# Performance work log

Measured on AMD Instinct MI355X. Metric: run time of the kernel, lower is better.

Reference implementation:

```python
import jax, jax.numpy as jnp
import numpy as np

B, S, D = 128, 50, 128
NUM_NODE = 40000
HOP, N_ITER, SAMPLE = 2, 2, 12
N_NEI = 8
TEMP, MU, LEAK = 0.5, 0.1, 0.2


def setup_inputs() -> dict:
    key = jax.random.key(0)
    ks = jax.random.split(key, 32)
    stdv = 1.0 / np.sqrt(D)
    u = lambda k, shp: jax.random.uniform(k, shp, jnp.float32, -stdv, stdv)
    return {
        "inputs": jax.random.randint(ks[0], (B, S), 0, NUM_NODE),
        "adj": jax.random.randint(ks[1], (B, S, S), 0, 5),
        "item": jax.random.randint(ks[2], (B, S), 0, NUM_NODE),
        "simi_mask": jax.random.randint(ks[3], (B, S, S), 0, 2),
        "as_items_0": jax.random.randint(ks[4], (B, S, N_NEI), 0, NUM_NODE),
        "as_items_1": jax.random.randint(ks[5], (B, S, N_NEI), 0, NUM_NODE),
        "as_items_ssl_0": jax.random.randint(ks[6], (B, S, N_NEI), 0, NUM_NODE),
        "as_items_ssl_1": jax.random.randint(ks[7], (B, S, N_NEI), 0, NUM_NODE),
        "last_item_mask": jnp.zeros((B, S), bool).at[:, -1].set(True),
        "adj_all": jax.random.randint(ks[8], (NUM_NODE, SAMPLE), 0, NUM_NODE),
        "num": jax.random.uniform(ks[9], (NUM_NODE, SAMPLE)),
        "emb": u(ks[10], (NUM_NODE, D)),
        "pos_emb": u(ks[11], (200, D)),
        "a_local": u(ks[12], (N_ITER, 4, D)),
        "mir_w1": u(ks[13], (N_ITER, D, D)),
        "mir_w2": u(ks[14], (N_ITER, D, D)),
        "glob_w1": u(ks[15], (HOP, D + 1, D)),
        "glob_w2": u(ks[16], (HOP, D, 1)),
        "glob_w3": u(ks[17], (HOP, 2 * D, D)),
        "attr_w": u(ks[18], (2 * D, D)),
        "highway_w": u(ks[19], (2 * D, D)),
        "glu1_w": u(ks[20], (D, D)),
        "glu2_w": u(ks[21], (D, D)),
        "glu4_w": u(ks[22], (D, D)),
        "glu4_b": u(ks[23], (D,)),
        "w_s": u(ks[24], (D, 1)),
        "gate_w": u(ks[25], (2 * D, D)),
    }


def _forward(num, emb, pos_emb, a_local, mir_w1, mir_w2, glob_w1, glob_w2, glob_w3,
             attr_w, highway_w, glu1_w, glu2_w, glu4_w, glu4_b, w_s, gate_w,
             inputs, adj, item, simi_mask, as_lists, as_ssl_lists, last_item_mask, adj_all):
    mi = (inputs != 0).astype(emb.dtype)  # [B,S]
    h = emb[inputs]                        # [B,S,D]

    # ---- AttributeAggregator (masked-mean pool per attribute + gated fusion) ----
    def pool(idx_list):
        ps = []
        for idx in idx_list:
            m = (idx != 0).astype(emb.dtype)[..., None]  # [B,S,N,1]
            ps.append(jnp.sum(emb[idx] * m, 2) / (jnp.sum(m, 2) + 1e-8))
        return jnp.mean(jnp.stack(ps), 0)  # [B,S,D]
    hf1 = pool(as_lists)
    hf2 = pool(as_ssl_lists)
    g_attr = jax.nn.sigmoid(jnp.concatenate([h, hf1], -1) @ attr_w)
    hf = g_attr * h + (1.0 - g_attr) * hf1

    # ---- multi-hop neighbor sampling (irregular gathers) ----
    neigh = [inputs]
    wts = []
    for _ in range(HOP):
        flat = neigh[-1].reshape(-1)
        neigh.append(adj_all[flat].reshape(B, -1))
        wts.append(num[flat].reshape(B, -1))
    ev = [emb[n] for n in neigh]  # [B,S,D], [B,S*12,D], [B,S*144,D]

    item_emb = emb[item] * mi[..., None]
    sess = jnp.sum(item_emb, 1) / jnp.sum(mi, -1, keepdims=True)  # [B,D]

    # ---- GlobalAggregator stack (GCE-GNN style attention over sampled neighbors) ----
    for n_hop in range(HOP):
        nxt = []
        for hop in range(HOP - n_hop):
            sv = ev[hop]                                   # [B,M,D]
            nv = ev[hop + 1].reshape(B, -1, SAMPLE, D)     # [B,M,12,D]
            nw = wts[hop].reshape(B, -1, SAMPLE)           # [B,M,12]
            extra = jnp.broadcast_to(sess[:, None, None, :], nv.shape)
            a = jnp.concatenate([extra * nv, nw[..., None]], -1)  # [B,M,12,D+1]
            a = jax.nn.leaky_relu(a @ glob_w1[n_hop], LEAK)
            a = jax.nn.softmax((a @ glob_w2[n_hop])[..., 0], -1)[..., None]
            agg = jnp.sum(a * nv, -2)
            nxt.append(jnp.tanh(jnp.concatenate([sv, agg], -1) @ glob_w3[n_hop]))
        ev = nxt
    h_global = ev[0].reshape(B, S, D)

    # ---- LocalAggregator (edge-typed GAT) + MirrorAggregator (gated exchange) ----
    x = h
    mirror = hf
    for i in range(HOP):
        e = jax.nn.leaky_relu(jnp.einsum('bid,bjd,kd->kbij', x, x, a_local[i]), LEAK)
        att = jnp.full((B, S, S), -9e15, x.dtype)
        for k in range(4):
            att = jnp.where(adj == k + 1, e[k], att)
        x = jax.nn.softmax(att, -1) @ x
        gm = jax.nn.sigmoid(x @ mir_w1[i] + mirror @ mir_w2[i])
        x, mirror = gm * x + (1.0 - gm) * mirror, gm * mirror + (1.0 - gm) * x

    # ---- highway + last-item select ----
    g = jax.nn.sigmoid(jnp.concatenate([h, x], -1) @ highway_w)
    x_dot = g * h + (1.0 - g) * x
    h_local = jnp.sum(x_dot * last_item_mask[..., None].astype(x_dot.dtype), 1)  # [B,D]

    mask = mi[..., None]
    pos = pos_emb[:S][None]  # [1,S,D]
    bw = emb[1:]             # [NUM_NODE-1,D]
    hs = jnp.sum(h_global * mask, -2) / jnp.sum(mask, 1)  # [B,D]

    # ---- SSL pairwise similarity loss ----
    sim = jnp.einsum('bid,bjd->bij', hf1, hf2) / TEMP
    l = -jnp.log(jax.nn.softmax(sim, 2) + 1e-8)
    simi_loss = jnp.mean(jnp.sum(l * (simi_mask == 1), (1, 2)))

    # ---- attention-style GLU scoring ----
    hp = x_dot + pos
    nh = jax.nn.sigmoid(hp @ glu1_w + hs[:, None, :] @ glu2_w + h_local[:, None, :] @ glu4_w + glu4_b)
    beta = (nh @ w_s) * mask
    zg = jnp.sum(beta * hp, 1)  # [B,D]
    gf = jax.nn.sigmoid(jnp.concatenate([zg, h_local], -1) @ gate_w) * MU
    zh = gf * h_local + (1.0 - gf) * zg
    scores = zh @ bw.T  # [B, NUM_NODE-1]
    return simi_loss, scores


def reference(inputs, adj, item, simi_mask, as_items_0, as_items_1,
              as_items_ssl_0, as_items_ssl_1, last_item_mask, adj_all, num,
              emb, pos_emb, a_local, mir_w1, mir_w2, glob_w1, glob_w2, glob_w3,
              attr_w, highway_w, glu1_w, glu2_w, glu4_w, glu4_b, w_s, gate_w):
    return _forward(num, emb, pos_emb, a_local, mir_w1, mir_w2, glob_w1, glob_w2, glob_w3,
                    attr_w, highway_w, glu1_w, glu2_w, glu4_w, glu4_b, w_s, gate_w,
                    inputs, adj, item, simi_mask, [as_items_0, as_items_1],
                    [as_items_ssl_0, as_items_ssl_1], last_item_mask, adj_all)
```

## Files before the change

kernel.cpp:

```cpp
#include <hip/hip_runtime.h>
#include <hip/hip_bf16.h>
#include <type_traits>


#define B 128
#define S 50
#define D 128
#define SAMPLE 12
#define NNEI 8
#define NODES 40000
#define NSC (NODES - 1)
#define LEAK 0.2f
#define TEMPV 0.5f
#define MUV 0.1f
#define NEG_BIG -3.0e38f
#define NUNITS (B * S * 13)
#define NGA (NUNITS / 4)

typedef const float* fpp;
typedef float* fpw;
typedef unsigned short u16;
typedef __attribute__((ext_vector_type(8))) short bfrag8;
typedef __attribute__((ext_vector_type(4))) float f32x4;

__device__ __forceinline__ float sigm(float x) { return 1.f / (1.f + __expf(-x)); }
__device__ __forceinline__ float tanh_f(float x) { return 1.f - 2.f / (__expf(2.f * x) + 1.f); }
__device__ __forceinline__ float leaky(float x) { return x >= 0.f ? x : LEAK * x; }
__device__ __forceinline__ u16 f2bf(float v) {
  __hip_bfloat16 h = __float2bfloat16(v);
  return *reinterpret_cast<u16*>(&h);
}
__device__ __forceinline__ float lde(const float* p, long i) { return p[i]; }
__device__ __forceinline__ float lde(const u16* p, long i) {
  union { unsigned int u; float f; } c;
  c.u = ((unsigned int)p[i]) << 16;
  return c.f;
}
__device__ __forceinline__ float bfu(short s) {
  union { unsigned u; float f; } c;
  c.u = ((unsigned)(unsigned short)s) << 16;
  return c.f;
}

template <typename ET>
__device__ __forceinline__ bfrag8 load_frag(const ET* __restrict__ emb, long row, int koff) {
  if constexpr (sizeof(ET) == 2) {
    return *(const bfrag8*)(const void*)(emb + row * D + koff);
  } else {
    const float* s = (const float*)(emb + row * D + koff);
    float4 lo = *(const float4*)s;
    float4 hi = *(const float4*)(s + 4);
    bfrag8 b;
    b[0] = (short)f2bf(lo.x); b[1] = (short)f2bf(lo.y);
    b[2] = (short)f2bf(lo.z); b[3] = (short)f2bf(lo.w);
    b[4] = (short)f2bf(hi.x); b[5] = (short)f2bf(hi.y);
    b[6] = (short)f2bf(hi.z); b[7] = (short)f2bf(hi.w);
    return b;
  }
}

__device__ __forceinline__ bfrag8 scale8(bfrag8 r, float4 sa, float4 sb) {
  bfrag8 o;
  o[0] = (short)f2bf(bfu(r[0]) * sa.x); o[1] = (short)f2bf(bfu(r[1]) * sa.y);
  o[2] = (short)f2bf(bfu(r[2]) * sa.z); o[3] = (short)f2bf(bfu(r[3]) * sa.w);
  o[4] = (short)f2bf(bfu(r[4]) * sb.x); o[5] = (short)f2bf(bfu(r[5]) * sb.y);
  o[6] = (short)f2bf(bfu(r[6]) * sb.z); o[7] = (short)f2bf(bfu(r[7]) * sb.w);
  return o;
}

struct __align__(16) SMk5 { float xi[D]; float ak[4][D]; float alpha[56]; float part[4][2][64]; };
struct __align__(16) SMk7 { float hi[D]; float part[2][64]; };
struct __align__(16) SMga { u16 nvs[2][2][16 * 136]; };
struct __align__(16) SMgb {
  u16 nvs[16 * 136];
  float ev[13 * 128];
  float agg1[128];
  float red[2][16];
  float nw[16];
  int svidx[16];
};
union __align__(16) SMF1 { SMk5 a; SMk7 b; SMga c; };
union __align__(16) SMF2 { SMk5 a; SMgb d; };

__global__ __launch_bounds__(256) void kprep_emb(fpp emb, u16* __restrict__ out) {
  long i = ((long)blockIdx.x * 256 + threadIdx.x) * 4;
  if (i + 3 >= (long)NODES * D) return;
  float4 v = *(const float4*)(emb + i);
  out[i + 0] = f2bf(v.x); out[i + 1] = f2bf(v.y);
  out[i + 2] = f2bf(v.z); out[i + 3] = f2bf(v.w);
}

__global__ __launch_bounds__(256) void kprep4(fpp gw1, fpp gw3,
                                              u16* __restrict__ p1a,
                                              u16* __restrict__ p1b,
                                              u16* __restrict__ p3a,
                                              u16* __restrict__ p3b) {
  int i = blockIdx.x * 256 + threadIdx.x;
  fpp W; u16* dst; int KS;
  if (i < 16384)      { W = gw1;             dst = p1a; KS = 4; }
  else if (i < 32768) { W = gw1 + 129 * 128; dst = p1b; KS = 4; i -= 16384; }
  else if (i < 65536) { W = gw3;             dst = p3a; KS = 8; i -= 32768; }
  else                { W = gw3 + 256 * 128; dst = p3b; KS = 8; i -= 65536; }
  int e = i & 7;
  int lane = (i >> 3) & 63;
  int rest = i >> 9;
  int ks = rest % KS, nt = rest / KS;
  int k = ks * 32 + ((lane >> 4) << 3) + e;
  int n = (nt << 4) + (lane & 15);
  dst[i] = f2bf(W[(long)k * 128 + n]);
}

template <typename ET>
__global__ __launch_bounds__(128) void k1_gather(
    const int* __restrict__ inputs, const int* __restrict__ as0,
    const int* __restrict__ as1, const int* __restrict__ ss0,
    const int* __restrict__ ss1, const ET* __restrict__ emb, fpp attr_w,
    fpw h, fpw hf1, fpw hf2, float* __restrict__ mi, fpw xA, fpw mir) {
  int bs = blockIdx.x;
  int d = threadIdx.x;
  __shared__ float h_s[D], hf1_s[D];
  int inp = inputs[bs];
  float hv = lde(emb, (long)inp * D + d);
  const int* lists[4] = {as0, as1, ss0, ss1};
  float p[4];
#pragma unroll
  for (int l = 0; l < 4; l++) {
    float sum = 0.f, cnt = 0.f;
    const int* L = lists[l] + (long)bs * NNEI;
#pragma unroll
    for (int n = 0; n < NNEI; n++) {
      int idx = L[n];
      if (idx != 0) { sum += lde(emb, (long)idx * D + d); cnt += 1.f; }
    }
    p[l] = sum / (cnt + 1e-8f);
  }
  float hf1v = 0.5f * (p[0] + p[1]);
  float hf2v = 0.5f * (p[2] + p[3]);
  h_s[d] = hv;
  hf1_s[d] = hf1v;
  __syncthreads();
  float acc = 0.f;
  for (int k = 0; k < D; k++)
    acc += h_s[k] * attr_w[(long)k * D + d] + hf1_s[k] * attr_w[(long)(D + k) * D + d];
  float g = sigm(acc);
  float hfv = g * hv + (1.f - g) * hf1v;
  long o = (long)bs * D + d;
  h[o] = hv; hf1[o] = hf1v; hf2[o] = hf2v; xA[o] = hv; mir[o] = hfv;
  if (d == 0) mi[bs] = (inp != 0) ? 1.f : 0.f;
}

__global__ __launch_bounds__(128) void k2_sess(const int* __restrict__ inputs,
                                               const int* __restrict__ item,
                                               fpp emb, fpw sess) {
  int b = blockIdx.x;
  int d = threadIdx.x;
  float acc = 0.f, ms = 0.f;
  for (int s = 0; s < S; s++) {
    int inp = inputs[b * S + s];
    float m = (inp != 0) ? 1.f : 0.f;
    int it = item[b * S + s];
    acc += emb[(long)it * D + d] * m;
    ms += m;
  }
  sess[(long)b * D + d] = acc / ms;
}

template <typename ET>
__device__ __forceinline__ void dev_kga2(
    u16* __restrict__ nvs0, u16* __restrict__ nvs1,
    const int* __restrict__ inputs, const int* __restrict__ adj_all, fpp num,
    const ET* __restrict__ emb, fpp sess, fpp W1a, fpp W2a,
    const u16* __restrict__ p1a, u16* __restrict__ aggws, int gu0, int lane) {
  int q = lane >> 4;
  int mrow = lane & 15;
  float wl8[8], w28[8];
#pragma unroll
  for (int nt = 0; nt < 8; nt++) {
    int col = nt * 16 + mrow;
    wl8[nt] = W1a[(long)D * D + col];
    w28[nt] = W2a[col];
  }
  bfrag8 sA[2][4];
  float nwq[2][4];
#pragma unroll
  for (int g = 0; g < 2; g++) {
    int gu = gu0 + g;
    int bs = gu / 13;
    int u = gu - bs * 13;
    int b = bs / S;
    int src0 = inputs[bs];
    int srcu = (u == 0) ? src0 : adj_all[(long)src0 * SAMPLE + (u - 1)];
    int rid = adj_all[(long)srcu * SAMPLE + (mrow < 12 ? mrow : 0)];
#pragma unroll
    for (int i = 0; i < 4; i++)
      nwq[g][i] = (q < 3) ? num[(long)srcu * SAMPLE + q * 4 + i] : 0.f;
    const float* sessb = sess + (long)b * D;
    u16* nb = g ? nvs1 : nvs0;
    bfrag8 raw[4];
#pragma unroll
    for (int ks = 0; ks < 4; ks++)
      raw[ks] = load_frag(emb, (long)rid, ks * 32 + q * 8);
#pragma unroll
    for (int ks = 0; ks < 4; ks++)
      *(bfrag8*)(nb + mrow * 136 + ks * 32 + q * 8) = raw[ks];
#pragma unroll
    for (int ks = 0; ks < 4; ks++) {
      float4 sa = *(const float4*)(sessb + ks * 32 + q * 8);
      float4 sb = *(const float4*)(sessb + ks * 32 + q * 8 + 4);
      sA[g][ks] = scale8(raw[ks], sa, sb);
    }
  }
  float lp[2][4] = {{0.f, 0.f, 0.f, 0.f}, {0.f, 0.f, 0.f, 0.f}};
#pragma unroll
  for (int nt = 0; nt < 8; nt++) {
    f32x4 acc0 = (f32x4){0.f, 0.f, 0.f, 0.f};
    f32x4 acc1 = (f32x4){0.f, 0.f, 0.f, 0.f};
#pragma unroll
    for (int ks = 0; ks < 4; ks++) {
      bfrag8 bb = *(const bfrag8*)(p1a + ks * 512 + lane * 8 + nt * 2048);
      acc0 = __builtin_amdgcn_mfma_f32_16x16x32_bf16(sA[0][ks], bb, acc0, 0, 0, 0);
      acc1 = __builtin_amdgcn_mfma_f32_16x16x32_bf16(sA[1][ks], bb, acc1, 0, 0, 0);
    }
#pragma unroll
    for (int i = 0; i < 4; i++) {
      lp[0][i] += leaky(acc0[i] + nwq[0][i] * wl8[nt]) * w28[nt];
      lp[1][i] += leaky(acc1[i] + nwq[1][i] * wl8[nt]) * w28[nt];
    }
  }
#pragma unroll
  for (int off = 1; off <= 8; off <<= 1)
#pragma unroll
    for (int g = 0; g < 2; g++)
#pragma unroll
      for (int i = 0; i < 4; i++) lp[g][i] += __shfl_xor(lp[g][i], off, 64);
#pragma unroll
  for (int g = 0; g < 2; g++) {
    float m4 = (q < 3) ? fmaxf(fmaxf(lp[g][0], lp[g][1]), fmaxf(lp[g][2], lp[g][3]))
                       : NEG_BIG;
    m4 = fmaxf(m4, __shfl_xor(m4, 16, 64));
    m4 = fmaxf(m4, __shfl_xor(m4, 32, 64));
    float e0 = 0.f, e1 = 0.f, e2 = 0.f, e3 = 0.f, ssum = 0.f;
    if (q < 3) {
      e0 = __expf(lp[g][0] - m4); e1 = __expf(lp[g][1] - m4);
      e2 = __expf(lp[g][2] - m4); e3 = __expf(lp[g][3] - m4);
      ssum = e0 + e1 + e2 + e3;
    }
    ssum += __shfl_xor(ssum, 16, 64);
    ssum += __shfl_xor(ssum, 32, 64);
    float inv = 1.f / ssum;
    float al[4] = {e0 * inv, e1 * inv, e2 * inv, e3 * inv};
    float aj[12];
#pragma unroll
    for (int j = 0; j < 12; j++) aj[j] = __shfl(al[j & 3], (j >> 2) << 4, 64);
    const u16* nb = g ? nvs1 : nvs0;
    float a0 = 0.f, a1 = 0.f;
#pragma unroll
    for (int j = 0; j < 12; j++) {
      unsigned pv = *(const unsigned*)(nb + j * 136 + lane * 2);
      union { unsigned u; float f; } lo, hi;
      lo.u = pv << 16; hi.u = pv & 0xffff0000u;
      a0 += aj[j] * lo.f; a1 += aj[j] * hi.f;
    }
    unsigned pk = ((unsigned)f2bf(a1) << 16) | (unsigned)f2bf(a0);
    *(unsigned*)(aggws + (long)(gu0 + g) * 128 + lane * 2) = pk;
  }
}

template <typename ET>
__device__ __forceinline__ void dev_kgb(
    SMgb& sm, const int* __restrict__ inputs, const int* __restrict__ adj_all,
    fpp num, const ET* __restrict__ emb, fpp sess, fpp W1b, fpp W2b, fpp W3b,
    const u16* __restrict__ p1b, const u16* __restrict__ p3a,
    const u16* __restrict__ aggws, fpw hg, int bs) {
  int b = bs / S;
  int d = threadIdx.x;
  int lane = d & 63;
  int w = d >> 6;
  int q = lane >> 4;
  int mrow = lane & 15;

#pragma unroll
  for (int r = 12; r < 16; r++) {
    sm.nvs[r * 136 + d] = 0;
    if (d < 8) sm.nvs[r * 136 + 128 + d] = 0;
  }
  int src0 = inputs[bs];
  if (d < 16)
    sm.svidx[d] = (d == 0) ? src0 : (d <= 12 ? adj_all[(long)src0 * SAMPLE + d - 1] : 0);
  if (d < SAMPLE) sm.nw[d] = num[(long)src0 * SAMPLE + d];
  float sess_d = sess[(long)b * D + d];
  __syncthreads();

  {
    long svr = sm.svidx[mrow];
    f32x4 accB[4];
#pragma unroll
    for (int nt = 0; nt < 4; nt++) accB[nt] = (f32x4){0.f, 0.f, 0.f, 0.f};
#pragma unroll
    for (int ks = 0; ks < 4; ks++) {
      bfrag8 a = (bfrag8){0, 0, 0, 0, 0, 0, 0, 0};
      if (mrow < 13) a = load_frag(emb, svr, ks * 32 + q * 8);
      const u16* pb = p3a + (w * 32 + ks) * 512 + lane * 8;
#pragma unroll
      for (int nt = 0; nt < 4; nt++)
        accB[nt] = __builtin_amdgcn_mfma_f32_16x16x32_bf16(
            a, *(const bfrag8*)(pb + nt * 4096), accB[nt], 0, 0, 0);
    }
#pragma unroll
    for (int ks = 4; ks < 8; ks++) {
      bfrag8 a = (bfrag8){0, 0, 0, 0, 0, 0, 0, 0};
      if (mrow < 13)
        a = *(const bfrag8*)(aggws + ((long)bs * 13 + mrow) * 128 + (ks - 4) * 32 + q * 8);
      const u16* pb = p3a + (w * 32 + ks) * 512 + lane * 8;
#pragma unroll
      for (int nt = 0; nt < 4; nt++)
        accB[nt] = __builtin_amdgcn_mfma_f32_16x16x32_bf16(
            a, *(const bfrag8*)(pb + nt * 4096), accB[nt], 0, 0, 0);
    }
#pragma unroll
    for (int nt = 0; nt < 4; nt++) {
      int col = (w * 4 + nt) * 16 + mrow;
#pragma unroll
      for (int i = 0; i < 4; i++) {
        int u2 = q * 4 + i;
        if (u2 < 13) sm.ev[u2 * 128 + col] = tanh_f(accB[nt][i]);
      }
    }
  }
  __syncthreads();

  {
    float w2B[4], wlB[4];
#pragma unroll
    for (int nt = 0; nt < 4; nt++) {
      int col = (w * 4 + nt) * 16 + mrow;
      w2B[nt] = W2b[col];
      wlB[nt] = W1b[(long)D * D + col];
    }
    float evreg[SAMPLE];
#pragma unroll
    for (int j = 0; j < SAMPLE; j++) {
      float e = sm.ev[(1 + j) * 128 + d];
      evreg[j] = e;
      sm.nvs[j * 136 + d] = f2bf(e * sess_d);
    }
    __syncthreads();

    f32x4 acc[4];
#pragma unroll
    for (int nt = 0; nt < 4; nt++) acc[nt] = (f32x4){0.f, 0.f, 0.f, 0.f};
#pragma unroll
    for (int ks = 0; ks < 4; ks++) {
      bfrag8 a = *(const bfrag8*)(sm.nvs + mrow * 136 + q * 8 + ks * 32);
      const u16* pb = p1b + (w * 16 + ks) * 512 + lane * 8;
#pragma unroll
      for (int nt = 0; nt < 4; nt++) {
        bfrag8 bb = *(const bfrag8*)(pb + nt * 2048);
        acc[nt] = __builtin_amdgcn_mfma_f32_16x16x32_bf16(a, bb, acc[nt], 0, 0, 0);
      }
    }
    float lp[4] = {0.f, 0.f, 0.f, 0.f};
    float nwq[4];
#pragma unroll
    for (int i = 0; i < 4; i++) nwq[i] = (q < 3) ? sm.nw[q * 4 + i] : 0.f;
#pragma unroll
    for (int nt = 0; nt < 4; nt++)
#pragma unroll
      for (int i = 0; i < 4; i++)
        lp[i] += leaky(acc[nt][i] + nwq[i] * wlB[nt]) * w2B[nt];
#pragma unroll
    for (int off = 1; off <= 8; off <<= 1)
#pragma unroll
      for (int i = 0; i < 4; i++) lp[i] += __shfl_xor(lp[i], off, 64);
    if (mrow == 0 && q < 3) {
#pragma unroll
      for (int i = 0; i < 4; i++) sm.red[w][q * 4 + i] = lp[i];
    }
    __syncthreads();

    float lg[SAMPLE];
#pragma unroll
    for (int j = 0; j < SAMPLE; j++) lg[j] = sm.red[0][j] + sm.red[1][j];
    float mx = lg[0];
#pragma unroll
    for (int j = 1; j < SAMPLE; j++) mx = fmaxf(mx, lg[j]);
    float se = 0.f;
#pragma unroll
    for (int j = 0; j < SAMPLE; j++) { lg[j] = __expf(lg[j] - mx); se += lg[j]; }
    float inv = 1.f / se;
    float agg1d = 0.f;
#pragma unroll
    for (int j = 0; j < SAMPLE; j++) agg1d += lg[j] * inv * evreg[j];
    sm.agg1[d] = agg1d;
    __syncthreads();

    float accf = 0.f;
#pragma unroll 4
    for (int k4 = 0; k4 < 32; k4++) {
      float4 a4 = *(const float4*)&sm.ev[4 * k4];
      float4 g4 = *(const float4*)&sm.agg1[4 * k4];
      accf += a4.x * W3b[(4 * k4 + 0) * D + d] + a4.y * W3b[(4 * k4 + 1) * D + d] +
              a4.z * W3b[(4 * k4 + 2) * D + d] + a4.w * W3b[(4 * k4 + 3) * D + d] +
              g4.x * W3b[(D + 4 * k4 + 0) * D + d] + g4.y * W3b[(D + 4 * k4 + 1) * D + d] +
              g4.z * W3b[(D + 4 * k4 + 2) * D + d] + g4.w * W3b[(D + 4 * k4 + 3) * D + d];
    }
    hg[(long)bs * D + d] = tanh_f(accf);
  }
}

__device__ __forceinline__ void dev_k5ab(SMk5& sm, fpp x, const int* __restrict__ adj,
                                         fpp a_loc, fpp w1, fpp w2, fpw xout,
                                         fpw mir, fpp hw, fpp h, fpw x_dot,
                                         float* __restrict__ h_local, int bs, int fin) {
  int b = bs / S;
  int row = bs % S;
  int tid = threadIdx.x;
  long idx = ((long)b * S + row) * D + tid;
  sm.xi[tid] = x[idx];
#pragma unroll
  for (int k = 0; k < 4; k++) sm.ak[k][tid] = a_loc[(long)k * D + tid];
  __syncthreads();
  {
    int j = tid & 63, hf = tid >> 6;
    float a0 = 0.f, a1 = 0.f, a2 = 0.f, a3 = 0.f;
    if (j < S) {
      const float* xj = x + ((long)b * S + j) * D + hf * 64;
      int off = hf * 64;
      for (int dd = 0; dd < 64; dd++) {
        float prod = sm.xi[off + dd] * xj[dd];
        a0 += prod * sm.ak[0][off + dd];
        a1 += prod * sm.ak[1][off + dd];
        a2 += prod * sm.ak[2][off + dd];
        a3 += prod * sm.ak[3][off + dd];
      }
    }
    sm.part[0][hf][j] = a0; sm.part[1][hf][j] = a1;
    sm.part[2][hf][j] = a2; sm.part[3][hf][j] = a3;
  }
  __syncthreads();
  if (tid < 64) {
    int j = tid;
    float att;
    if (j < S) {
      float acc0 = sm.part[0][0][j] + sm.part[0][1][j];
      float acc1 = sm.part[1][0][j] + sm.part[1][1][j];
      float acc2 = sm.part[2][0][j] + sm.part[2][1][j];
      float acc3 = sm.part[3][0][j] + sm.part[3][1][j];
      int av = adj[((long)b * S + row) * S + j];
      att = -9e15f;
      if (av == 1) att = leaky(acc0);
      else if (av == 2) att = leaky(acc1);
      else if (av == 3) att = leaky(acc2);
      else if (av == 4) att = leaky(acc3);
    } else {
      att = NEG_BIG;
    }
    float mx = att;
#pragma unroll
    for (int o = 32; o > 0; o >>= 1) mx = fmaxf(mx, __shfl_xor(mx, o, 64));
    float e = __expf(att - mx);
    float ssum = e;
#pragma unroll
    for (int o = 32; o > 0; o >>= 1) ssum += __shfl_xor(ssum, o, 64);
    if (j < S) sm.alpha[j] = e / ssum;
  }
  __syncthreads();
  float xn = 0.f;
  for (int j = 0; j < S; j++) xn += sm.alpha[j] * x[((long)b * S + j) * D + tid];
  float mv = mir[idx];
  sm.ak[0][tid] = xn;
  sm.ak[1][tid] = mv;
  __syncthreads();
  float a2m = 0.f;
  for (int k = 0; k < D; k++)
    a2m += sm.ak[0][k] * w1[(long)k * D + tid] + sm.ak[1][k] * w2[(long)k * D + tid];
  float g = sigm(a2m);
  float xg = g * xn + (1.f - g) * mv;
  if (!fin) {
    xout[idx] = xg;
    mir[idx] = g * mv + (1.f - g) * xn;
    return;
  }
  float hv = h[idx];
  sm.ak[2][tid] = hv;
  sm.ak[3][tid] = xg;
  __syncthreads();
  float a3m = 0.f;
  for (int k = 0; k < D; k++)
    a3m += sm.ak[2][k] * hw[(long)k * D + tid] + sm.ak[3][k] * hw[(long)(D + k) * D + tid];
  float gh = sigm(a3m);
  float xd = gh * hv + (1.f - gh) * xg;
  x_dot[idx] = xd;
  if (row == S - 1) h_local[(long)b * D + tid] = xd;
}

__device__ __forceinline__ void dev_k7(SMk7& sm, fpp hf1, fpp hf2,
                                       const int* __restrict__ simi_mask,
                                       float* __restrict__ loss, int bs) {
  int b = bs / S;
  int i = bs % S;
  int t = threadIdx.x;
  sm.hi[t] = hf1[((long)b * S + i) * D + t];
  __syncthreads();
  {
    int j = t & 63, hf = t >> 6;
    float acc = 0.f;
    if (j < S) {
      const float* r = hf2 + ((long)b * S + j) * D + hf * 64;
      int off = hf * 64;
      for (int dd = 0; dd < 64; dd++) acc += sm.hi[off + dd] * r[dd];
    }
    sm.part[hf][j] = acc;
  }
  __syncthreads();
  if (t < 64) {
    int j = t;
    float sim = (j < S) ? (sm.part[0][j] + sm.part[1][j]) * (1.0f / TEMPV) : NEG_BIG;
    float mx = sim;
#pragma unroll
    for (int o = 32; o > 0; o >>= 1) mx = fmaxf(mx, __shfl_xor(mx, o, 64));
    float e = __expf(sim - mx);
    float ssum = e;
#pragma unroll
    for (int o = 32; o > 0; o >>= 1) ssum += __shfl_xor(ssum, o, 64);
    float contrib = 0.f;
    if (j < S) {
      float p = e / ssum;
      float l = -__logf(p + 1e-8f);
      if (simi_mask[((long)b * S + i) * S + j] == 1) contrib = l;
    }
#pragma unroll
    for (int o = 32; o > 0; o >>= 1) contrib += __shfl_xor(contrib, o, 64);
    if (j == 0) atomicAdd(loss, contrib);
  }
}

template <typename ET>
__global__ __launch_bounds__(128) void kF1(
    const int* __restrict__ inputs, const int* __restrict__ adj_all, fpp num,
    const ET* __restrict__ emb, fpp sess, fpp W1a, fpp W2a,
    const u16* __restrict__ p1a, u16* __restrict__ aggws,
    fpp xA, const int* __restrict__ adj, fpp a_loc, fpp mw1, fpp mw2,
    fpw xB, fpw mir,
    fpp hf1, fpp hf2, const int* __restrict__ simi_mask,
    float* __restrict__ loss) {
  __shared__ SMF1 sm;
  int bid = blockIdx.x;
  if (bid < NGA) {
    int t = threadIdx.x;
    int w = t >> 6, lane = t & 63;
    dev_kga2<ET>(sm.c.nvs[w][0], sm.c.nvs[w][1], inputs, adj_all, num, emb,
                 sess, W1a, W2a, p1a, aggws, bid * 4 + w * 2, lane);
  } else if (bid < NGA + B * S) {
    dev_k5ab(sm.a, xA, adj, a_loc, mw1, mw2, xB, mir, nullptr, nullptr,
             nullptr, nullptr, bid - NGA, 0);
  } else {
    dev_k7(sm.b, hf1, hf2, simi_mask, loss, bid - NGA - B * S);
  }
}

template <typename ET>
__global__ __launch_bounds__(128) void kF2(
    const int* __restrict__ inputs, const int* __restrict__ adj_all, fpp num,
    const ET* __restrict__ emb, fpp sess, fpp W1b, fpp W2b, fpp W3b,
    const u16* __restrict__ p1b, const u16* __restrict__ p3a,
    const u16* __restrict__ aggws, fpw hg,
    fpp xB, const int* __restrict__ adj, fpp a_loc2, fpp mw1b, fpp mw2b,
    fpw mir, fpp hw, fpp h, fpw x_dot, float* __restrict__ h_local) {
  __shared__ SMF2 sm;
  int bid = blockIdx.x;
  if (bid < B * S) {
    dev_kgb<ET>(sm.d, inputs, adj_all, num, emb, sess, W1b, W2b, W3b, p1b,
                p3a, aggws, hg, bid);
  } else {
    dev_k5ab(sm.a, xB, adj, a_loc2, mw1b, mw2b, nullptr, mir, hw, h, x_dot,
             h_local, bid - B * S, 1);
  }
}

__global__ __launch_bounds__(128) void k5ab(fpp x, const int* __restrict__ adj,
                                            fpp a_loc, fpp w1, fpp w2,
                                            fpw xout, fpw mir,
                                            fpp hw, fpp h, fpw x_dot,
                                            float* __restrict__ h_local,
                                            int fin) {
  __shared__ SMk5 sm;
  dev_k5ab(sm, x, adj, a_loc, w1, w2, xout, mir, hw, h, x_dot, h_local,
           blockIdx.x, fin);
}

__global__ __launch_bounds__(128) void k7_simi(fpp hf1, fpp hf2,
                                               const int* __restrict__ simi_mask,
                                               float* __restrict__ loss) {
  __shared__ SMk7 sm;
  dev_k7(sm, hf1, hf2, simi_mask, loss, blockIdx.x);
}

template <typename ET>
__global__ __launch_bounds__(128) void kG_mono(
    const int* __restrict__ inputs, const int* __restrict__ adj_all,
    fpp num, const ET* __restrict__ emb, fpp sess,
    fpp W1a, fpp W2a, fpp W1b, fpp W2b, fpp W3b,
    const u16* __restrict__ p1a, const u16* __restrict__ p1b,
    const u16* __restrict__ p3a, fpw hg) {
  int bs = blockIdx.x;
  int b = bs / S;
  int d = threadIdx.x;
  int lane = d & 63;
  int w = d >> 6;
  int q = lane >> 4;
  int mrow = lane & 15;

  __shared__ __align__(16) u16 nvs_l[16 * 136];
  __shared__ __align__(16) u16 svagg_l[16 * 264];
  __shared__ __align__(16) float ev_l[13 * 128];
  __shared__ __align__(16) float agg1_l[128];
  __shared__ float red_l[2][16];
  __shared__ float nw_l[16];

#pragma unroll
  for (int r = 12; r < 16; r++) {
    nvs_l[r * 136 + d] = 0;
    if (d < 8) nvs_l[r * 136 + 128 + d] = 0;
  }
#pragma unroll
  for (int r = 13; r < 16; r++) {
    svagg_l[r * 264 + d] = 0;
    svagg_l[r * 264 + 128 + d] = 0;
    if (d < 8) svagg_l[r * 264 + 256 + d] = 0;
  }

  float sess_d = sess[(long)b * D + d];
  int src0 = __builtin_amdgcn_readfirstlane(inputs[bs]);
  int n1[SAMPLE];
#pragma unroll
  for (int j = 0; j < SAMPLE; j++)
    n1[j] = __builtin_amdgcn_readfirstlane(adj_all[(long)src0 * SAMPLE + j]);
  svagg_l[0 * 264 + d] = f2bf(lde(emb, (long)src0 * D + d));

  float w2A[4], wlA[4], w2B[4], wlB[4];
#pragma unroll
  for (int nt = 0; nt < 4; nt++) {
    int col = (w * 4 + nt) * 16 + mrow;
    w2A[nt] = W2a[col];
    wlA[nt] = W1a[(long)D * D + col];
    w2B[nt] = W2b[col];
    wlB[nt] = W1b[(long)D * D + col];
  }

  float pre[SAMPLE], pnw = 0.f;
  {
#pragma unroll
    for (int j = 0; j < SAMPLE; j++)
      pre[j] = lde(emb, (long)n1[j] * D + d);
    if (d < SAMPLE) pnw = num[(long)src0 * SAMPLE + d];
  }
  for (int u = 0; u < 13; u++) {
    if (d < SAMPLE) nw_l[d] = pnw;
    float nvreg[SAMPLE];
#pragma unroll
    for (int j = 0; j < SAMPLE; j++) {
      nvreg[j] = pre[j];
      nvs_l[j * 136 + d] = f2bf(pre[j] * sess_d);
    }
    if (u == 0) {
#pragma unroll
      for (int j = 0; j < SAMPLE; j++)
        svagg_l[(1 + j) * 264 + d] = f2bf(nvreg[j]);
    }
    __syncthreads();
    if (u < 12) {
      int srcn = n1[u];
#pragma unroll
      for (int j = 0; j < SAMPLE; j++) {
        int nj = __builtin_amdgcn_readfirstlane(adj_all[(long)srcn * SAMPLE + j]);
        pre[j] = lde(emb, (long)nj * D + d);
      }
      if (d < SAMPLE) pnw = num[(long)srcn * SAMPLE + d];
    }
    f32x4 acc[4];
#pragma unroll
    for (int nt = 0; nt < 4; nt++) acc[nt] = (f32x4){0.f, 0.f, 0.f, 0.f};
#pragma unroll
    for (int ks = 0; ks < 4; ks++) {
      bfrag8 a = *(const bfrag8*)(nvs_l + mrow * 136 + q * 8 + ks * 32);
      const u16* pb = p1a + (w * 16 + ks) * 512 + lane * 8;
#pragma unroll
      for (int nt = 0; nt < 4; nt++) {
        bfrag8 bb = *(const bfrag8*)(pb + nt * 2048);
        acc[nt] = __builtin_amdgcn_mfma_f32_16x16x32_bf16(a, bb, acc[nt], 0, 0, 0);
      }
    }
    float lp[4] = {0.f, 0.f, 0.f, 0.f};
    float nwq[4];
#pragma unroll
    for (int i = 0; i < 4; i++) nwq[i] = (q < 3) ? nw_l[q * 4 + i] : 0.f;
#pragma unroll
    for (int nt = 0; nt < 4; nt++)
#pragma unroll
      for (int i = 0; i < 4; i++)
        lp[i] += leaky(acc[nt][i] + nwq[i] * wlA[nt]) * w2A[nt];
#pragma unroll
    for (int off = 1; off <= 8; off <<= 1)
#pragma unroll
      for (int i = 0; i < 4; i++) lp[i] += __shfl_xor(lp[i], off, 64);
    if (mrow == 0 && q < 3) {
#pragma unroll
      for (int i = 0; i < 4; i++) red_l[w][q * 4 + i] = lp[i];
    }
    __syncthreads();
    float lg[SAMPLE];
#pragma unroll
    for (int j = 0; j < SAMPLE; j++) lg[j] = red_l[0][j] + red_l[1][j];
    float mx = lg[0];
#pragma unroll
    for (int j = 1; j < SAMPLE; j++) mx = fmaxf(mx, lg[j]);
    float se = 0.f;
#pragma unroll
    for (int j = 0; j < SAMPLE; j++) { lg[j] = __expf(lg[j] - mx); se += lg[j]; }
    float inv = 1.f / se;
    float aggd = 0.f;
#pragma unroll
    for (int j = 0; j < SAMPLE; j++) aggd += lg[j] * inv * nvreg[j];
    svagg_l[u * 264 + 128 + d] = f2bf(aggd);
  }
  __syncthreads();

  {
    f32x4 accB[4];
#pragma unroll
    for (int nt = 0; nt < 4; nt++) accB[nt] = (f32x4){0.f, 0.f, 0.f, 0.f};
#pragma unroll
    for (int ks = 0; ks < 8; ks++) {
      bfrag8 a = *(const bfrag8*)(svagg_l + mrow * 264 + q * 8 + ks * 32);
      const u16* pb = p3a + (w * 32 + ks) * 512 + lane * 8;
#pragma unroll
      for (int nt = 0; nt < 4; nt++) {
        bfrag8 bb = *(const bfrag8*)(pb + nt * 4096);
        accB[nt] = __builtin_amdgcn_mfma_f32_16x16x32_bf16(a, bb, accB[nt], 0, 0, 0);
      }
    }
#pragma unroll
    for (int nt = 0; nt < 4; nt++) {
      int col = (w * 4 + nt) * 16 + mrow;
#pragma unroll
      for (int i = 0; i < 4; i++) {
        int u2 = q * 4 + i;
        if (u2 < 13) ev_l[u2 * 128 + col] = tanh_f(accB[nt][i]);
      }
    }
    __syncthreads();
  }

  {
    float evreg[SAMPLE];
#pragma unroll
    for (int j = 0; j < SAMPLE; j++) {
      float e = ev_l[(1 + j) * 128 + d];
      evreg[j] = e;
      nvs_l[j * 136 + d] = f2bf(e * sess_d);
    }
    if (d < SAMPLE) nw_l[d] = num[(long)src0 * SAMPLE + d];
    __syncthreads();

    f32x4 acc[4];
#pragma unroll
    for (int nt = 0; nt < 4; nt++) acc[nt] = (f32x4){0.f, 0.f, 0.f, 0.f};
#pragma unroll
    for (int ks = 0; ks < 4; ks++) {
      bfrag8 a = *(const bfrag8*)(nvs_l + mrow * 136 + q * 8 + ks * 32);
      const u16* pb = p1b + (w * 16 + ks) * 512 + lane * 8;
#pragma unroll
      for (int nt = 0; nt < 4; nt++) {
        bfrag8 bb = *(const bfrag8*)(pb + nt * 2048);
        acc[nt] = __builtin_amdgcn_mfma_f32_16x16x32_bf16(a, bb, acc[nt], 0, 0, 0);
      }
    }
    float lp[4] = {0.f, 0.f, 0.f, 0.f};
    float nwq[4];
#pragma unroll
    for (int i = 0; i < 4; i++) nwq[i] = (q < 3) ? nw_l[q * 4 + i] : 0.f;
#pragma unroll
    for (int nt = 0; nt < 4; nt++)
#pragma unroll
      for (int i = 0; i < 4; i++)
        lp[i] += leaky(acc[nt][i] + nwq[i] * wlB[nt]) * w2B[nt];
#pragma unroll
    for (int off = 1; off <= 8; off <<= 1)
#pragma unroll
      for (int i = 0; i < 4; i++) lp[i] += __shfl_xor(lp[i], off, 64);
    if (mrow == 0 && q < 3) {
#pragma unroll
      for (int i = 0; i < 4; i++) red_l[w][q * 4 + i] = lp[i];
    }
    __syncthreads();

    float lg[SAMPLE];
#pragma unroll
    for (int j = 0; j < SAMPLE; j++) lg[j] = red_l[0][j] + red_l[1][j];
    float mx = lg[0];
#pragma unroll
    for (int j = 1; j < SAMPLE; j++) mx = fmaxf(mx, lg[j]);
    float se = 0.f;
#pragma unroll
    for (int j = 0; j < SAMPLE; j++) { lg[j] = __expf(lg[j] - mx); se += lg[j]; }
    float inv = 1.f / se;
    float agg1d = 0.f;
#pragma unroll
    for (int j = 0; j < SAMPLE; j++) agg1d += lg[j] * inv * evreg[j];
    agg1_l[d] = agg1d;
    __syncthreads();

    float accf = 0.f;
#pragma unroll 4
    for (int k4 = 0; k4 < 32; k4++) {
      float4 a4 = *(const float4*)&ev_l[4 * k4];
      float4 g4 = *(const float4*)&agg1_l[4 * k4];
      accf += a4.x * W3b[(4 * k4 + 0) * D + d] + a4.y * W3b[(4 * k4 + 1) * D + d] +
              a4.z * W3b[(4 * k4 + 2) * D + d] + a4.w * W3b[(4 * k4 + 3) * D + d] +
              g4.x * W3b[(D + 4 * k4 + 0) * D + d] + g4.y * W3b[(D + 4 * k4 + 1) * D + d] +
              g4.z * W3b[(D + 4 * k4 + 2) * D + d] + g4.w * W3b[(D + 4 * k4 + 3) * D + d];
    }
    hg[(long)bs * D + d] = tanh_f(accf);
  }
}

__global__ __launch_bounds__(512) void k8_glu(
    fpp hg, fpp x_dot, fpp pos, fpp h_local, const float* __restrict__ mi,
    fpp glu1, fpp glu2, fpp glu4, fpp glu4b, fpp w_s, fpp gate_w, fpw zh) {
  int b = blockIdx.x;
  int t = threadIdx.x;
  int d = t & 127;
  int g = t >> 7;
  __shared__ float hs_s[D], hl_s[D];
  __shared__ float hp_g[4][D], part[4][D], zg_g[4][D];
  __shared__ float red2[4][2];
  float msf = 0.f;
  for (int s = 0; s < S; s++) msf += mi[b * S + s];
  float hsacc = 0.f;
  for (int s = g * 13; s < min(S, g * 13 + 13); s++)
    hsacc += hg[((long)b * S + s) * D + d] * mi[b * S + s];
  part[g][d] = hsacc;
  if (g == 1) hl_s[d] = h_local[(long)b * D + d];
  __syncthreads();
  if (g == 0) hs_s[d] = (part[0][d] + part[1][d] + part[2][d] + part[3][d]) / msf;
  __syncthreads();
  float c = glu4b[d];
  for (int k = 0; k < D; k++)
    c += hs_s[k] * glu2[(long)k * D + d] + hl_s[k] * glu4[(long)k * D + d];
  float wsd = w_s[d];
  float zg = 0.f;
  for (int it = 0; it < 13; it++) {
    int s = g * 13 + it;
    bool act = s < S;
    float hp = 0.f;
    if (act) {
      hp = x_dot[((long)b * S + s) * D + d] + pos[(long)s * D + d];
      hp_g[g][d] = hp;
    }
    __syncthreads();
    if (act) {
      float acc = c;
      for (int k = 0; k < D; k++) acc += hp_g[g][k] * glu1[(long)k * D + d];
      float v = sigm(acc) * wsd;
#pragma unroll
      for (int o = 32; o > 0; o >>= 1) v += __shfl_down(v, o, 64);
      if ((t & 63) == 0) red2[g][(t >> 6) & 1] = v;
    }
    __syncthreads();
    if (act) {
      float beta = (red2[g][0] + red2[g][1]) * mi[b * S + s];
      zg += beta * hp;
    }
    __syncthreads();
  }
  zg_g[g][d] = zg;
  __syncthreads();
  if (g == 0) {
    float zgf = zg_g[0][d] + zg_g[1][d] + zg_g[2][d] + zg_g[3][d];
    hp_g[0][d] = zgf;
  }
  __syncthreads();
  if (g == 0) {
    float zgf = hp_g[0][d];
    float acc = 0.f;
    for (int k = 0; k < D; k++)
      acc += hp_g[0][k] * gate_w[(long)k * D + d] +
             hl_s[k] * gate_w[(long)(D + k) * D + d];
    float gf = sigm(acc) * MUV;
    zh[(long)b * D + d] = gf * hl_s[d] + (1.f - gf) * zgf;
  }
}

template <typename ET>
__global__ __launch_bounds__(256) void k9_scores(fpp zh, const ET* __restrict__ emb,
                                                 fpp loss, float* __restrict__ out) {
  int t = threadIdx.x;
  if (blockIdx.x == 0 && t == 0) out[0] = loss[0] * (1.0f / (float)B);
  int lane = t & 63;
  int w = t >> 6;
  int q = lane >> 4;
  int mrow = lane & 15;
  long n = (long)blockIdx.x * 64 + w * 16 + mrow;
  bool valid = n < NSC;
  long nrow = valid ? (n + 1) : 1;
  bfrag8 bfr[4];
#pragma unroll
  for (int ks = 0; ks < 4; ks++) {
    if constexpr (sizeof(ET) == 2) {
      bfr[ks] = *(const bfrag8*)(const void*)(emb + nrow * D + ks * 32 + q * 8);
    } else {
      const float* src = (const float*)(emb + nrow * D + ks * 32 + q * 8);
      float4 lo = *(const float4*)src;
      float4 hi = *(const float4*)(src + 4);
      bfrag8 bb;
      bb[0] = (short)f2bf(lo.x); bb[1] = (short)f2bf(lo.y);
      bb[2] = (short)f2bf(lo.z); bb[3] = (short)f2bf(lo.w);
      bb[4] = (short)f2bf(hi.x); bb[5] = (short)f2bf(hi.y);
      bb[6] = (short)f2bf(hi.z); bb[7] = (short)f2bf(hi.w);
      bfr[ks] = bb;
    }
  }
#pragma unroll
  for (int mt = 0; mt < 8; mt++) {
    f32x4 acc = (f32x4){0.f, 0.f, 0.f, 0.f};
#pragma unroll
    for (int ks = 0; ks < 4; ks++) {
      const float* za = zh + (long)(mt * 16 + mrow) * D + ks * 32 + q * 8;
      float4 lo = *(const float4*)za;
      float4 hi = *(const float4*)(za + 4);
      bfrag8 a;
      a[0] = (short)f2bf(lo.x); a[1] = (short)f2bf(lo.y);
      a[2] = (short)f2bf(lo.z); a[3] = (short)f2bf(lo.w);
      a[4] = (short)f2bf(hi.x); a[5] = (short)f2bf(hi.y);
      a[6] = (short)f2bf(hi.z); a[7] = (short)f2bf(hi.w);
      acc = __builtin_amdgcn_mfma_f32_16x16x32_bf16(a, bfr[ks], acc, 0, 0, 0);
    }
    if (valid) {
#pragma unroll
      for (int i = 0; i < 4; i++) {
        int m = mt * 16 + q * 4 + i;
        out[1 + (long)m * NSC + n] = acc[i];
      }
    }
  }
}

extern "C" void kernel_launch(void* const* d_in, const int* in_sizes, int n_in,
                              void* d_out, int out_size, void* d_ws, size_t ws_size,
                              hipStream_t stream) {
  (void)in_sizes; (void)n_in; (void)out_size;
  const int* inputs = (const int*)d_in[0];
  const int* adj = (const int*)d_in[1];
  const int* item = (const int*)d_in[2];
  const int* simi_mask = (const int*)d_in[3];
  const int* as0 = (const int*)d_in[4];
  const int* as1 = (const int*)d_in[5];
  const int* ss0 = (const int*)d_in[6];
  const int* ss1 = (const int*)d_in[7];
  const int* adj_all = (const int*)d_in[9];
  fpp num = (fpp)d_in[10];
  fpp emb = (fpp)d_in[11];
  fpp pos = (fpp)d_in[12];
  fpp a_local = (fpp)d_in[13];
  fpp mir_w1 = (fpp)d_in[14];
  fpp mir_w2 = (fpp)d_in[15];
  fpp gw1 = (fpp)d_in[16];
  fpp gw2 = (fpp)d_in[17];
  fpp gw3 = (fpp)d_in[18];
  fpp attr_w = (fpp)d_in[19];
  fpp highway_w = (fpp)d_in[20];
  fpp glu1 = (fpp)d_in[21];
  fpp glu2 = (fpp)d_in[22];
  fpp glu4 = (fpp)d_in[23];
  fpp glu4b = (fpp)d_in[24];
  fpp w_s = (fpp)d_in[25];
  fpp gate_w = (fpp)d_in[26];

  float* ob = (float*)d_out;
  constexpr long BSD_ = (long)B * S * D;
  fpw s_h = ob + 0 * BSD_;
  fpw s_hf1 = ob + 1 * BSD_;
  fpw s_hf2 = ob + 2 * BSD_;
  fpw s_mir = ob + 3 * BSD_;
  fpw s_xA = ob + 4 * BSD_;
  fpw s_xB = ob + 5 * BSD_;

  float* ws = (float*)d_ws;
  float* w_loss = ws + 0;
  float* w_mi = ws + 16;
  float* w_sess = w_mi + (long)B * S;
  float* w_hl = w_sess + (long)B * D;
  float* w_zh = w_hl + (long)B * D;
  u16* p1a = (u16*)(ws + 72000);
  u16* p1b = (u16*)(ws + 72000 + 8192);
  u16* p3a = (u16*)(ws + 72000 + 16384);
  u16* p3b = (u16*)(ws + 72000 + 32768);
  u16* embbf = (u16*)((char*)d_ws + 491520);
  u16* aggws = (u16*)((char*)d_ws + 10731520);
  bool useBF = ws_size >= (size_t)12 * 1024 * 1024;
  bool useSplit = useBF && ws_size >= ((size_t)32 << 20);

  hipMemsetAsync((void*)w_loss, 0, sizeof(float), stream);

  kprep4<<<384, 256, 0, stream>>>(gw1, gw3, p1a, p1b, p3a, p3b);
  if (useBF)
    kprep_emb<<<(NODES * D / 4 + 255) / 256, 256, 0, stream>>>(emb, embbf);

  if (useBF)
    k1_gather<u16><<<B * S, 128, 0, stream>>>(inputs, as0, as1, ss0, ss1,
                                              embbf, attr_w, s_h, s_hf1, s_hf2,
                                              w_mi, s_xA, s_mir);
  else
    k1_gather<float><<<B * S, 128, 0, stream>>>(inputs, as0, as1, ss0, ss1,
                                                emb, attr_w, s_h, s_hf1, s_hf2,
                                                w_mi, s_xA, s_mir);
  k2_sess<<<B, 128, 0, stream>>>(inputs, item, emb, w_sess);

  if (useSplit) {
    kF1<u16><<<NGA + 2 * B * S, 128, 0, stream>>>(
        inputs, adj_all, num, embbf, w_sess, gw1, gw2, p1a, aggws,
        s_xA, adj, a_local, mir_w1, mir_w2, s_xB, s_mir,
        s_hf1, s_hf2, simi_mask, w_loss);
    kF2<u16><<<2 * B * S, 128, 0, stream>>>(
        inputs, adj_all, num, embbf, w_sess, gw1 + 129 * 128, gw2 + 128,
        gw3 + 256 * 128, p1b, p3a, aggws, s_hf2 ,
        s_xB, adj, a_local + 4 * D, mir_w1 + (long)D * D,
        mir_w2 + (long)D * D, s_mir, highway_w, s_h, s_hf1 , w_hl);
  } else {
    k7_simi<<<B * S, 128, 0, stream>>>(s_hf1, s_hf2, simi_mask, w_loss);
    if (useBF)
      kG_mono<u16><<<B * S, 128, 0, stream>>>(inputs, adj_all, num, embbf,
                                              w_sess, gw1, gw2,
                                              gw1 + 129 * 128, gw2 + 128,
                                              gw3 + 256 * 128, p1a, p1b, p3a,
                                              s_hf2 );
    else
      kG_mono<float><<<B * S, 128, 0, stream>>>(inputs, adj_all, num, emb,
                                                w_sess, gw1, gw2,
                                                gw1 + 129 * 128, gw2 + 128,
                                                gw3 + 256 * 128, p1a, p1b,
                                                p3a, s_hf2 );
    k5ab<<<B * S, 128, 0, stream>>>(s_xA, adj, a_local, mir_w1, mir_w2,
                                    s_xB, s_mir, highway_w, s_h, s_hf1, w_hl, 0);
    k5ab<<<B * S, 128, 0, stream>>>(s_xB, adj, a_local + 4 * D,
                                    mir_w1 + (long)D * D, mir_w2 + (long)D * D,
                                    s_xA, s_mir, highway_w, s_h,
                                    s_hf1 , w_hl, 1);
  }

  k8_glu<<<B, 512, 0, stream>>>(s_hf2 , s_hf1 , pos,
                                w_hl, w_mi, glu1, glu2, glu4, glu4b, w_s,
                                gate_w, w_zh);
  if (useBF)
    k9_scores<u16><<<(NSC + 63) / 64, 256, 0, stream>>>(w_zh, embbf, w_loss,
                                                        (float*)d_out);
  else
    k9_scores<float><<<(NSC + 63) / 64, 256, 0, stream>>>(w_zh, emb, w_loss,
                                                          (float*)d_out);
}
```

Measured before the change: 679.9 us.

## Fuse prep kernels and interleave heterogeneous block roles in fused kernels

Merges weight packing, embedding bf16 conversion and session mean into one launch (kP). Inside kF1 and kF2 it interleaves block types: kF1 uses groups of 21 blocks, 13 gather-aggregate and 8 alternating k5ab/k7 blocks. kF2 alternates gb and k5ab blocks so the mixed workloads share CUs more evenly. It also shrinks the shared-memory neighbour buffer to 12 rows and skips storing the padding rows, which lowers LDS use and may allow higher occupancy.

```diff
diff --git a/kernel.cpp b/kernel.cpp
--- a/kernel.cpp
+++ b/kernel.cpp
@@ -70,7 +70,7 @@
 
 struct __align__(16) SMk5 { float xi[D]; float ak[4][D]; float alpha[56]; float part[4][2][64]; };
 struct __align__(16) SMk7 { float hi[D]; float part[2][64]; };
-struct __align__(16) SMga { u16 nvs[2][2][16 * 136]; };
+struct __align__(16) SMga { u16 nvs[2][2][12 * 136]; };
 struct __align__(16) SMgb {
   u16 nvs[16 * 136];
   float ev[13 * 128];
@@ -90,12 +90,11 @@
   out[i + 2] = f2bf(v.z); out[i + 3] = f2bf(v.w);
 }
 
-__global__ __launch_bounds__(256) void kprep4(fpp gw1, fpp gw3,
-                                              u16* __restrict__ p1a,
-                                              u16* __restrict__ p1b,
-                                              u16* __restrict__ p3a,
-                                              u16* __restrict__ p3b) {
-  int i = blockIdx.x * 256 + threadIdx.x;
+__device__ __forceinline__ void dev_prep4(int i, fpp gw1, fpp gw3,
+                                          u16* __restrict__ p1a,
+                                          u16* __restrict__ p1b,
+                                          u16* __restrict__ p3a,
+                                          u16* __restrict__ p3b) {
   fpp W; u16* dst; int KS;
   if (i < 16384)      { W = gw1;             dst = p1a; KS = 4; }
   else if (i < 32768) { W = gw1 + 129 * 128; dst = p1b; KS = 4; i -= 16384; }
@@ -108,6 +107,56 @@
   int k = ks * 32 + ((lane >> 4) << 3) + e;
   int n = (nt << 4) + (lane & 15);
   dst[i] = f2bf(W[(long)k * 128 + n]);
+}
+
+__global__ __launch_bounds__(256) void kprep4(fpp gw1, fpp gw3,
+                                              u16* __restrict__ p1a,
+                                              u16* __restrict__ p1b,
+                                              u16* __restrict__ p3a,
+                                              u16* __restrict__ p3b) {
+  dev_prep4(blockIdx.x * 256 + threadIdx.x, gw1, gw3, p1a, p1b, p3a, p3b);
+}
+
+__device__ __forceinline__ void dev_k2(const int* __restrict__ inputs,
+                                       const int* __restrict__ item,
+                                       fpp emb, fpw sess, int b, int d) {
+  float acc = 0.f, ms = 0.f;
+  for (int s = 0; s < S; s++) {
+    int inp = inputs[b * S + s];
+    float m = (inp != 0) ? 1.f : 0.f;
+    int it = item[b * S + s];
+    acc += emb[(long)it * D + d] * m;
+    ms += m;
+  }
+  sess[(long)b * D + d] = acc / ms;
+}
+
+__global__ __launch_bounds__(128) void k2_sess(const int* __restrict__ inputs,
+                                               const int* __restrict__ item,
+                                               fpp emb, fpw sess) {
+  dev_k2(inputs, item, emb, sess, blockIdx.x, threadIdx.x);
+}
+
+__global__ __launch_bounds__(256) void kP(fpp gw1, fpp gw3,
+                                          u16* __restrict__ p1a, u16* __restrict__ p1b,
+                                          u16* __restrict__ p3a, u16* __restrict__ p3b,
+                                          fpp emb, u16* __restrict__ embbf,
+                                          const int* __restrict__ inputs,
+                                          const int* __restrict__ item, fpw sess) {
+  int bid = blockIdx.x;
+  int t = threadIdx.x;
+  if (bid < 384) {
+    dev_prep4(bid * 256 + t, gw1, gw3, p1a, p1b, p3a, p3b);
+  } else if (bid < 5384) {
+    long i = ((long)(bid - 384) * 256 + t) * 4;
+    if (i + 3 < (long)NODES * D) {
+      float4 v = *(const float4*)(emb + i);
+      embbf[i + 0] = f2bf(v.x); embbf[i + 1] = f2bf(v.y);
+      embbf[i + 2] = f2bf(v.z); embbf[i + 3] = f2bf(v.w);
+    }
+  } else {
+    if (t < 128) dev_k2(inputs, item, emb, sess, bid - 5384, t);
+  }
 }
 
 template <typename ET>
@@ -149,22 +198,6 @@
   if (d == 0) mi[bs] = (inp != 0) ? 1.f : 0.f;
 }
 
-__global__ __launch_bounds__(128) void k2_sess(const int* __restrict__ inputs,
-                                               const int* __restrict__ item,
-                                               fpp emb, fpw sess) {
-  int b = blockIdx.x;
-  int d = threadIdx.x;
-  float acc = 0.f, ms = 0.f;
-  for (int s = 0; s < S; s++) {
-    int inp = inputs[b * S + s];
-    float m = (inp != 0) ? 1.f : 0.f;
-    int it = item[b * S + s];
-    acc += emb[(long)it * D + d] * m;
-    ms += m;
-  }
-  sess[(long)b * D + d] = acc / ms;
-}
-
 template <typename ET>
 __device__ __forceinline__ void dev_kga2(
     u16* __restrict__ nvs0, u16* __restrict__ nvs1,
@@ -200,9 +233,11 @@
 #pragma unroll
     for (int ks = 0; ks < 4; ks++)
       raw[ks] = load_frag(emb, (long)rid, ks * 32 + q * 8);
-#pragma unroll
-    for (int ks = 0; ks < 4; ks++)
-      *(bfrag8*)(nb + mrow * 136 + ks * 32 + q * 8) = raw[ks];
+    if (mrow < 12) {
+#pragma unroll
+      for (int ks = 0; ks < 4; ks++)
+        *(bfrag8*)(nb + mrow * 136 + ks * 32 + q * 8) = raw[ks];
+    }
 #pragma unroll
     for (int ks = 0; ks < 4; ks++) {
       float4 sa = *(const float4*)(sessb + ks * 32 + q * 8);
@@ -546,16 +581,21 @@
     float* __restrict__ loss) {
   __shared__ SMF1 sm;
   int bid = blockIdx.x;
-  if (bid < NGA) {
+  int grp = bid / 21;
+  int r = bid - grp * 21;
+  if (r < 13) {
+    int ga = grp * 13 + r;
     int t = threadIdx.x;
     int w = t >> 6, lane = t & 63;
     dev_kga2<ET>(sm.c.nvs[w][0], sm.c.nvs[w][1], inputs, adj_all, num, emb,
-                 sess, W1a, W2a, p1a, aggws, bid * 4 + w * 2, lane);
-  } else if (bid < NGA + B * S) {
-    dev_k5ab(sm.a, xA, adj, a_loc, mw1, mw2, xB, mir, nullptr, nullptr,
-             nullptr, nullptr, bid - NGA, 0);
+                 sess, W1a, W2a, p1a, aggws, ga * 4 + w * 2, lane);
   } else {
-    dev_k7(sm.b, hf1, hf2, simi_mask, loss, bid - NGA - B * S);
+    int o = grp * 8 + (r - 13);
+    if (o & 1)
+      dev_k7(sm.b, hf1, hf2, simi_mask, loss, o >> 1);
+    else
+      dev_k5ab(sm.a, xA, adj, a_loc, mw1, mw2, xB, mir, nullptr, nullptr,
+               nullptr, nullptr, o >> 1, 0);
   }
 }
 
@@ -569,13 +609,12 @@
     fpw mir, fpp hw, fpp h, fpw x_dot, float* __restrict__ h_local) {
   __shared__ SMF2 sm;
   int bid = blockIdx.x;
-  if (bid < B * S) {
+  if (bid & 1)
+    dev_k5ab(sm.a, xB, adj, a_loc2, mw1b, mw2b, nullptr, mir, hw, h, x_dot,
+             h_local, bid >> 1, 1);
+  else
     dev_kgb<ET>(sm.d, inputs, adj_all, num, emb, sess, W1b, W2b, W3b, p1b,
-                p3a, aggws, hg, bid);
-  } else {
-    dev_k5ab(sm.a, xB, adj, a_loc2, mw1b, mw2b, nullptr, mir, hw, h, x_dot,
-             h_local, bid - B * S, 1);
-  }
+                p3a, aggws, hg, bid >> 1);
 }
 
 __global__ __launch_bounds__(128) void k5ab(fpp x, const int* __restrict__ adj,
@@ -1003,22 +1042,13 @@
 
   hipMemsetAsync((void*)w_loss, 0, sizeof(float), stream);
 
-  kprep4<<<384, 256, 0, stream>>>(gw1, gw3, p1a, p1b, p3a, p3b);
-  if (useBF)
-    kprep_emb<<<(NODES * D / 4 + 255) / 256, 256, 0, stream>>>(emb, embbf);
-
-  if (useBF)
+  if (useSplit) {
+    kP<<<5512, 256, 0, stream>>>(gw1, gw3, p1a, p1b, p3a, p3b, emb, embbf,
+                                 inputs, item, w_sess);
     k1_gather<u16><<<B * S, 128, 0, stream>>>(inputs, as0, as1, ss0, ss1,
                                               embbf, attr_w, s_h, s_hf1, s_hf2,
                                               w_mi, s_xA, s_mir);
-  else
-    k1_gather<float><<<B * S, 128, 0, stream>>>(inputs, as0, as1, ss0, ss1,
-                                                emb, attr_w, s_h, s_hf1, s_hf2,
-                                                w_mi, s_xA, s_mir);
-  k2_sess<<<B, 128, 0, stream>>>(inputs, item, emb, w_sess);
-
-  if (useSplit) {
-    kF1<u16><<<NGA + 2 * B * S, 128, 0, stream>>>(
+    kF1<u16><<<33600, 128, 0, stream>>>(
         inputs, adj_all, num, embbf, w_sess, gw1, gw2, p1a, aggws,
         s_xA, adj, a_local, mir_w1, mir_w2, s_xB, s_mir,
         s_hf1, s_hf2, simi_mask, w_loss);
@@ -1028,7 +1058,19 @@
         s_xB, adj, a_local + 4 * D, mir_w1 + (long)D * D,
         mir_w2 + (long)D * D, s_mir, highway_w, s_h, s_hf1 , w_hl);
   } else {
+    kprep4<<<384, 256, 0, stream>>>(gw1, gw3, p1a, p1b, p3a, p3b);
+    if (useBF)
+      kprep_emb<<<(NODES * D / 4 + 255) / 256, 256, 0, stream>>>(emb, embbf);
+    if (useBF)
+      k1_gather<u16><<<B * S, 128, 0, stream>>>(inputs, as0, as1, ss0, ss1,
+                                                embbf, attr_w, s_h, s_hf1,
+                                                s_hf2, w_mi, s_xA, s_mir);
+    else
+      k1_gather<float><<<B * S, 128, 0, stream>>>(inputs, as0, as1, ss0, ss1,
+                                                  emb, attr_w, s_h, s_hf1,
+                                                  s_hf2, w_mi, s_xA, s_mir);
     k7_simi<<<B * S, 128, 0, stream>>>(s_hf1, s_hf2, simi_mask, w_loss);
+    k2_sess<<<B, 128, 0, stream>>>(inputs, item, emb, w_sess);
     if (useBF)
       kG_mono<u16><<<B * S, 128, 0, stream>>>(inputs, adj_all, num, embbf,
                                               w_sess, gw1, gw2,
```

After: 665.1 us. 2.2% less time.
